# Kernel optimization log

Measured on AMD Instinct MI355X. Metric: run time of the kernel, lower is better.

## Reference

```python
import jax, jax.numpy as jnp
import numpy as np
import math

N, Tp1, V = 256, 33, 10000
D_FEAT, H, W_DIM = 1280, 512, 256
NULL_IDX = 0


def setup_inputs() -> dict:
    key = jax.random.key(0)
    ks = jax.random.split(key, 10)
    feats = jax.random.normal(ks[0], (N, D_FEAT, 4, 4), dtype=jnp.float32)
    captions = jax.random.randint(ks[1], (N, Tp1), 0, V)
    W_proj = jax.random.normal(ks[2], (D_FEAT, H), dtype=jnp.float32) / math.sqrt(D_FEAT)
    b_proj = jnp.zeros((H,), dtype=jnp.float32)
    W_embed = jax.random.normal(ks[3], (V, W_DIM), dtype=jnp.float32) / math.sqrt(V)
    Wx = jax.random.normal(ks[4], (W_DIM, 4 * H), dtype=jnp.float32) / math.sqrt(W_DIM)
    Wh = jax.random.normal(ks[5], (H, 4 * H), dtype=jnp.float32) / math.sqrt(H)
    Wattn = jax.random.normal(ks[6], (H, 4 * H), dtype=jnp.float32) / math.sqrt(H)
    b = jnp.zeros((4 * H,), dtype=jnp.float32)
    W_vocab = jax.random.normal(ks[7], (H, V), dtype=jnp.float32) / math.sqrt(H)
    b_vocab = jnp.zeros((V,), dtype=jnp.float32)
    return {"feats": feats, "captions": captions, "W_proj": W_proj, "b_proj": b_proj,
            "W_embed": W_embed, "Wx": Wx, "Wh": Wh, "Wattn": Wattn, "b": b,
            "W_vocab": W_vocab, "b_vocab": b_vocab}


def _attention_lstm(x, A_flat, h0, Wx, Wh, Wattn, b):
    # x: (N,T,W), A_flat: (N,H,16), h0: (N,H)
    Hh = h0.shape[1]
    scale = 1.0 / math.sqrt(Hh)

    def step(carry, x_t):
        h, c = carry
        # scaled dot-product attention over the 16 spatial positions
        scores = jnp.einsum('nh,nhp->np', h, A_flat) * scale       # (N,16)
        w = jax.nn.softmax(scores, axis=1)
        attn = jnp.einsum('nhp,np->nh', A_flat, w)                 # (N,H)
        a = x_t @ Wx + h @ Wh + b + attn @ Wattn                   # (N,4H)
        i = jax.nn.sigmoid(a[:, 0:Hh])
        f = jax.nn.sigmoid(a[:, Hh:2 * Hh])
        o = jax.nn.sigmoid(a[:, 2 * Hh:3 * Hh])
        g = jnp.tanh(a[:, 3 * Hh:4 * Hh])
        c_next = f * c + i * g
        h_next = o * jnp.tanh(c_next)
        return (h_next, c_next), h_next

    (_, _), hs = jax.lax.scan(step, (h0, h0), jnp.swapaxes(x, 0, 1))
    return jnp.swapaxes(hs, 0, 1)  # (N,T,H)


def reference(feats, captions, W_proj, b_proj, W_embed, Wx, Wh, Wattn, b, W_vocab, b_vocab):
    cap_in = captions[:, :-1]   # (N,T)
    cap_out = captions[:, 1:]   # (N,T)
    # project CNN features per spatial location: (N,Dfeat,4,4) -> (N,H,4,4)
    A = jnp.einsum('ncij,ch->nhij', feats, W_proj) + b_proj[None, :, None, None]
    h0 = A.mean(axis=(2, 3))                     # (N,H); c0 = h0
    A_flat = A.reshape(A.shape[0], A.shape[1], 16)
    x = W_embed[cap_in]                           # (N,T,W)
    h = _attention_lstm(x, A_flat, h0, Wx, Wh, Wattn, b)
    scores = jnp.einsum('nth,hv->ntv', h, W_vocab) + b_vocab   # (N,T,V)
    # temporal softmax loss, sum over tokens (ignoring NULL), averaged over N
    logp = jax.nn.log_softmax(scores, axis=-1)
    nll = -jnp.take_along_axis(logp, cap_out[..., None], axis=-1)[..., 0]  # (N,T)
    mask = (cap_out != NULL_IDX).astype(scores.dtype)
    loss = jnp.sum(nll * mask) / scores.shape[0]
    return loss
```

## Files before the change

### kernel.cpp

```cpp
#include <hip/hip_runtime.h>
#include <hip/hip_bf16.h>

#define NB   256
#define NT   32
#define NV   10000
#define NVP  10240
#define NDF  1280
#define NH   512
#define VT_N 40

typedef short bf16x8 __attribute__((ext_vector_type(8)));
typedef float f32x4  __attribute__((ext_vector_type(4)));
typedef unsigned short u16;

__device__ __forceinline__ float b2f(u16 u) {
    union { unsigned i; float f; } v; v.i = ((unsigned)u) << 16; return v.f;
}
__device__ __forceinline__ u16 f2b(float f) {
    union { float f; unsigned i; } v; v.f = f;
    unsigned r = v.i + 0x7FFF + ((v.i >> 16) & 1);
    return (u16)(r >> 16);
}

__device__ __forceinline__ void gload16(const u16* g, u16* l) {
    __builtin_amdgcn_global_load_lds(
        (const __attribute__((address_space(1))) void*)g,
        (__attribute__((address_space(3))) void*)l, 16, 0, 0);
}

static const size_t B_C     = 0;
static const size_t B_SCP   = B_C     + (size_t)256*512*4;
static const size_t B_PMAX  = B_SCP   + (size_t)2*32*256*16*4;
static const size_t B_PSUM  = B_PMAX  + (size_t)8192*VT_N*4;
static const size_t B_TGT   = B_PSUM  + (size_t)8192*VT_N*4;
static const size_t B_LOSS  = B_TGT   + (size_t)8192*4;
static const size_t B_AB    = B_LOSS  + 16;
static const size_t B_XPB   = B_AB    + (size_t)256*16*512*2;
static const size_t B_HALLB = B_XPB   + (size_t)32*256*2048*2;
static const size_t B_WVT   = B_HALLB + (size_t)32*256*512*2;
static const size_t B_WXT   = B_WVT   + (size_t)10240*512*2;
static const size_t B_WHAT  = B_WXT   + (size_t)2048*256*2;
static const size_t B_HB0   = B_WHAT  + (size_t)2048*1024*2;
static const size_t B_HB1   = B_HB0   + (size_t)256*512*2;
static const size_t B_PREAW = B_HB1   + (size_t)256*512*2;

__global__ __launch_bounds__(256) void tconv_kernel(
    const float* __restrict__ src, u16* __restrict__ dst,
    int K, int N, int Npad, int ldK, int koff)
{
    __shared__ u16 tile[64][65];
    const int k0 = blockIdx.y * 64, n0 = blockIdx.x * 64, tid = threadIdx.x;
#pragma unroll
    for (int i = 0; i < 16; i++) {
        int idx = tid + i * 256;
        int kk = idx >> 6, nn = idx & 63;
        int n = n0 + nn;
        float v = (n < N) ? src[(size_t)(k0 + kk) * N + n] : 0.f;
        tile[kk][nn] = f2b(v);
    }
    __syncthreads();
#pragma unroll
    for (int i = 0; i < 16; i++) {
        int idx = tid + i * 256;
        int nn = idx >> 6, kk = idx & 63;
        int n = n0 + nn;
        if (n < Npad) dst[(size_t)n * ldK + koff + k0 + kk] = tile[kk][nn];
    }
}

__global__ __launch_bounds__(256) void ftrans_kernel(
    const float* __restrict__ feats, u16* __restrict__ fT)
{
    const int cch = blockIdx.x, n = blockIdx.y, tid = threadIdx.x;
    __shared__ u16 lt[64][17];
    const int c0 = cch * 64;
    const int c = tid >> 2, p4 = (tid & 3) * 4;
    float4 v = *(const float4*)(feats + (size_t)n * 20480 + (size_t)(c0 + c) * 16 + p4);
    lt[c][p4] = f2b(v.x); lt[c][p4 + 1] = f2b(v.y);
    lt[c][p4 + 2] = f2b(v.z); lt[c][p4 + 3] = f2b(v.w);
    __syncthreads();
    const int p = tid >> 4, cg = tid & 15;
    ushort4 o;
    o.x = lt[cg * 4 + 0][p]; o.y = lt[cg * 4 + 1][p];
    o.z = lt[cg * 4 + 2][p]; o.w = lt[cg * 4 + 3][p];
    *(ushort4*)(fT + (size_t)(n * 16 + p) * 1280 + c0 + cg * 4) = o;
}

__global__ __launch_bounds__(256) void proj_gemm_kernel(
    const u16* __restrict__ fT, const u16* __restrict__ WpT,
    const float* __restrict__ bp, u16* __restrict__ Ab)
{
    const int ct = blockIdx.x, rt = blockIdx.y;
    const int tid = threadIdx.x, w = tid >> 6, lane = tid & 63;
    const int r0 = rt * 64;
    const int lm = lane & 15, lkq = lane >> 4, lk = lkq * 8;
    const int nbase = ct * 128 + w * 32;

    f32x4 acc[4][2];
#pragma unroll
    for (int mt = 0; mt < 4; mt++)
#pragma unroll
        for (int nt = 0; nt < 2; nt++) acc[mt][nt] = (f32x4){0.f, 0.f, 0.f, 0.f};

    for (int kc = 0; kc < 1280; kc += 32) {
        bf16x8 af[4];
#pragma unroll
        for (int mt = 0; mt < 4; mt++)
            af[mt] = *(const bf16x8*)(fT + (size_t)(r0 + mt * 16 + lm) * 1280 + kc + lk);
#pragma unroll
        for (int nt = 0; nt < 2; nt++) {
            bf16x8 bfg = *(const bf16x8*)(WpT + (size_t)(nbase + nt * 16 + lm) * 1280 + kc + lk);
#pragma unroll
            for (int mt = 0; mt < 4; mt++)
                acc[mt][nt] = __builtin_amdgcn_mfma_f32_16x16x32_bf16(af[mt], bfg, acc[mt][nt], 0, 0, 0);
        }
    }
    float bbv[2];
#pragma unroll
    for (int nt = 0; nt < 2; nt++) bbv[nt] = bp[nbase + nt * 16 + lm];
#pragma unroll
    for (int mt = 0; mt < 4; mt++)
#pragma unroll
        for (int nt = 0; nt < 2; nt++)
#pragma unroll
            for (int r = 0; r < 4; r++) {
                int row = r0 + mt * 16 + lkq * 4 + r;
                int col = nbase + nt * 16 + lm;
                Ab[(size_t)row * 512 + col] = f2b(acc[mt][nt][r] + bbv[nt]);
            }
}

__global__ __launch_bounds__(256) void projmean_kernel(
    const u16* __restrict__ Ab, float* __restrict__ c0, u16* __restrict__ hb0)
{
    const int n = blockIdx.x, tid = threadIdx.x;
    const int col0 = tid, col1 = tid + 256;
    float s0 = 0.f, s1 = 0.f;
#pragma unroll
    for (int p = 0; p < 16; p++) {
        const u16* ap = Ab + ((size_t)n * 16 + p) * 512;
        s0 += b2f(ap[col0]);
        s1 += b2f(ap[col1]);
    }
    s0 *= 0.0625f; s1 *= 0.0625f;
    c0[n * 512 + col0] = s0;  c0[n * 512 + col1] = s1;
    hb0[(size_t)n * 512 + col0] = f2b(s0);
    hb0[(size_t)n * 512 + col1] = f2b(s1);
}

__global__ __launch_bounds__(256) void xp_mfma_kernel(
    const int* __restrict__ caps, const float* __restrict__ We,
    const u16* __restrict__ Wxt, const float* __restrict__ bb,
    u16* __restrict__ xpb)
{
    const int ct = blockIdx.x, rt = blockIdx.y;
    const int tid = threadIdx.x, w = tid >> 6, lane = tid & 63;
    const int r0 = rt * 64;
    const int lm = lane & 15, lkq = lane >> 4, lk = lkq * 8;
    const int nbase = ct * 512 + w * 128;

    int capm[4];
#pragma unroll
    for (int mt = 0; mt < 4; mt++) {
        int row = r0 + mt * 16 + lm;
        capm[mt] = caps[(row >> 5) * 33 + (row & 31)];
    }
    f32x4 acc[4][8];
#pragma unroll
    for (int mt = 0; mt < 4; mt++)
#pragma unroll
        for (int nt = 0; nt < 8; nt++) acc[mt][nt] = (f32x4){0.f, 0.f, 0.f, 0.f};

    for (int kc = 0; kc < 256; kc += 32) {
        bf16x8 af[4];
#pragma unroll
        for (int mt = 0; mt < 4; mt++) {
            const float* ap = We + (size_t)capm[mt] * 256 + kc + lk;
            float4 f0 = *(const float4*)ap;
            float4 f1 = *(const float4*)(ap + 4);
            bf16x8 t;
            t[0] = (short)f2b(f0.x); t[1] = (short)f2b(f0.y);
            t[2] = (short)f2b(f0.z); t[3] = (short)f2b(f0.w);
            t[4] = (short)f2b(f1.x); t[5] = (short)f2b(f1.y);
            t[6] = (short)f2b(f1.z); t[7] = (short)f2b(f1.w);
            af[mt] = t;
        }
#pragma unroll
        for (int nt = 0; nt < 8; nt++) {
            bf16x8 bfg = *(const bf16x8*)(Wxt + (size_t)(nbase + nt * 16 + lm) * 256 + kc + lk);
#pragma unroll
            for (int mt = 0; mt < 4; mt++)
                acc[mt][nt] = __builtin_amdgcn_mfma_f32_16x16x32_bf16(af[mt], bfg, acc[mt][nt], 0, 0, 0);
        }
    }
    float bbv[8];
#pragma unroll
    for (int nt = 0; nt < 8; nt++) bbv[nt] = bb[nbase + nt * 16 + lm];
#pragma unroll
    for (int mt = 0; mt < 4; mt++)
#pragma unroll
        for (int nt = 0; nt < 8; nt++)
#pragma unroll
            for (int r = 0; r < 4; r++) {
                int row = r0 + mt * 16 + lkq * 4 + r;
                int col = nbase + nt * 16 + lm;
                float v = acc[mt][nt][r] + bbv[nt];
                xpb[((size_t)(row & 31) * 256 + (row >> 5)) * 2048 + col] = f2b(v);
            }
}

__global__ __launch_bounds__(256) void preaw_mfma_kernel(
    const u16* __restrict__ Ab, const u16* __restrict__ what,
    u16* __restrict__ preaw)
{
    const int ct = blockIdx.x, rt = blockIdx.y;
    const int tid = threadIdx.x, w = tid >> 6, lane = tid & 63;
    const int r0 = rt * 64;
    const int lm = lane & 15, lkq = lane >> 4, lk = lkq * 8;
    const int nbase = ct * 512 + w * 128;

    f32x4 acc[4][8];
#pragma unroll
    for (int mt = 0; mt < 4; mt++)
#pragma unroll
        for (int nt = 0; nt < 8; nt++) acc[mt][nt] = (f32x4){0.f, 0.f, 0.f, 0.f};

    for (int kc = 0; kc < 512; kc += 32) {
        bf16x8 af[4];
#pragma unroll
        for (int mt = 0; mt < 4; mt++)
            af[mt] = *(const bf16x8*)(Ab + (size_t)(r0 + mt * 16 + lm) * 512 + kc + lk);
#pragma unroll
        for (int nt = 0; nt < 8; nt++) {
            bf16x8 bfg = *(const bf16x8*)(what + (size_t)(nbase + nt * 16 + lm) * 1024 + 512 + kc + lk);
#pragma unroll
            for (int mt = 0; mt < 4; mt++)
                acc[mt][nt] = __builtin_amdgcn_mfma_f32_16x16x32_bf16(af[mt], bfg, acc[mt][nt], 0, 0, 0);
        }
    }
#pragma unroll
    for (int mt = 0; mt < 4; mt++) {
        int nIdx = (r0 >> 4) + mt;
#pragma unroll
        for (int nt = 0; nt < 8; nt++) {
            int col = nbase + nt * 16 + lm;
            ushort4 o;
            o.x = f2b(acc[mt][nt][0]); o.y = f2b(acc[mt][nt][1]);
            o.z = f2b(acc[mt][nt][2]); o.w = f2b(acc[mt][nt][3]);
            *(ushort4*)(preaw + (size_t)nIdx * 32768 + (size_t)col * 16 + lkq * 4) = o;
        }
    }
}

__global__ __launch_bounds__(64) void score_init_kernel(
    const u16* __restrict__ hb0, const u16* __restrict__ Ab,
    float* __restrict__ scp)
{
    const int n = blockIdx.x, lane = threadIdx.x;
    const u16* hp = hb0 + (size_t)n * 512 + lane * 8;
    ushort4 h0 = *(const ushort4*)hp, h1 = *(const ushort4*)(hp + 4);
    float hv0 = b2f(h0.x), hv1 = b2f(h0.y), hv2 = b2f(h0.z), hv3 = b2f(h0.w);
    float hv4 = b2f(h1.x), hv5 = b2f(h1.y), hv6 = b2f(h1.z), hv7 = b2f(h1.w);
    float mine = 0.f;
#pragma unroll
    for (int p = 0; p < 16; p++) {
        const u16* ap = Ab + (size_t)n * 8192 + p * 512 + lane * 8;
        ushort4 a0 = *(const ushort4*)ap, a1 = *(const ushort4*)(ap + 4);
        float s = hv0*b2f(a0.x) + hv1*b2f(a0.y) + hv2*b2f(a0.z) + hv3*b2f(a0.w)
                + hv4*b2f(a1.x) + hv5*b2f(a1.y) + hv6*b2f(a1.z) + hv7*b2f(a1.w);
#pragma unroll
        for (int mask = 1; mask <= 32; mask <<= 1) s += __shfl_xor(s, mask, 64);
        if (lane == p) mine = s;
    }
    if (lane < 16) scp[n * 16 + lane] = mine;
    for (int i = lane; i < 31 * 16; i += 64)
        scp[(1 + (i >> 4)) * 4096 + n * 16 + (i & 15)] = 0.f;
}

__global__ __launch_bounds__(256, 2) void gates_fused_kernel(
    const u16* __restrict__ hb_in, const float* __restrict__ scp_in,
    const u16* __restrict__ what, const u16* __restrict__ preaw,
    const u16* __restrict__ xpt, const u16* __restrict__ Ab,
    float* __restrict__ c, u16* __restrict__ hb_out,
    u16* __restrict__ hallbt, float* __restrict__ scp_out)
{
    const int rt = blockIdx.x, cg = blockIdx.y;
    const int tid = threadIdx.x, ty = tid >> 6, lane = tid & 63;
    const int lm = lane & 15, lkq = lane >> 4, lk = lkq * 8;
    const int r0 = rt * 16, hc0 = cg * 16;

    __shared__ u16 hs[16 * 520];
    __shared__ float sred[16][17];
    __shared__ float wts[16][17];
    __shared__ float gred[4][16][18];
    __shared__ u16 hnew[16][16];

    const int col = ty * 512 + hc0 + lm;

    const u16* brow = what + (size_t)col * 1024 + lk;
    bf16x8 bfa[16];
#pragma unroll
    for (int i = 0; i < 16; i++) bfa[i] = *(const bf16x8*)(brow + i * 32);

    ushort4 pwv[4][4];
#pragma unroll
    for (int r = 0; r < 4; r++) {
        const u16* pp = preaw + (size_t)(r0 + lkq * 4 + r) * 32768 + (size_t)col * 16;
#pragma unroll
        for (int j = 0; j < 4; j++) pwv[r][j] = *(const ushort4*)(pp + j * 4);
    }
    u16 xpw[4];
#pragma unroll
    for (int r = 0; r < 4; r++) xpw[r] = xpt[(size_t)(r0 + lkq * 4 + r) * 2048 + col];

    const int rg = lkq * 4 + ty;
    const int idxg = (r0 + rg) * 512 + hc0 + lm;
    float cin = c[idxg];

    const int rs = tid >> 4, ps = tid & 15;
    ushort4 abv[4];
    {
        const u16* ap = Ab + (size_t)(r0 + rs) * 8192 + ps * 512 + hc0;
#pragma unroll
        for (int j = 0; j < 4; j++) abv[j] = *(const ushort4*)(ap + j * 4);
    }

#pragma unroll
    for (int i = 0; i < 8; i++) {
        int fid = tid + i * 256;
        int rr = fid >> 7, c4 = fid & 127;
        *(ushort4*)&hs[rr * 520 + c4 * 4] =
            *(const ushort4*)(hb_in + (size_t)(r0 + rr) * 512 + c4 * 4);
    }
    {
        float s = 0.f;
#pragma unroll
        for (int g = 0; g < 32; g++) s += scp_in[g * 4096 + (r0 + rs) * 16 + ps];
        sred[rs][ps] = s * 0.04419417382415922f;
    }
    __syncthreads();
    {
        float m = -1e30f;
#pragma unroll
        for (int q = 0; q < 16; q++) m = fmaxf(m, sred[rs][q]);
        float su = 0.f;
#pragma unroll
        for (int q = 0; q < 16; q++) su += __expf(sred[rs][q] - m);
        wts[rs][ps] = __expf(sred[rs][ps] - m) / su;
    }
    f32x4 acc = (f32x4){0.f, 0.f, 0.f, 0.f};
    const u16* arow = &hs[lm * 520 + lk];
#pragma unroll
    for (int i = 0; i < 16; i++) {
        bf16x8 af = *(const bf16x8*)(arow + i * 32);
        acc = __builtin_amdgcn_mfma_f32_16x16x32_bf16(af, bfa[i], acc, 0, 0, 0);
    }
    __syncthreads();
#pragma unroll
    for (int r = 0; r < 4; r++) {
        const int rl = lkq * 4 + r;
        float s = acc[r] + b2f(xpw[r]);
#pragma unroll
        for (int j = 0; j < 4; j++) {
            s += wts[rl][j * 4 + 0] * b2f(pwv[r][j].x);
            s += wts[rl][j * 4 + 1] * b2f(pwv[r][j].y);
            s += wts[rl][j * 4 + 2] * b2f(pwv[r][j].z);
            s += wts[rl][j * 4 + 3] * b2f(pwv[r][j].w);
        }
        gred[ty][rl][lm] = s;
    }
    __syncthreads();
    {
        float ai  = gred[0][rg][lm];
        float af_ = gred[1][rg][lm];
        float ao  = gred[2][rg][lm];
        float ag  = gred[3][rg][lm];
        float ig = 1.f / (1.f + __expf(-ai));
        float fg = 1.f / (1.f + __expf(-af_));
        float og = 1.f / (1.f + __expf(-ao));
        float gv = tanhf(ag);
        float cn = fg * cin + ig * gv;
        float hn = og * tanhf(cn);
        c[idxg] = cn;
        u16 hbv = f2b(hn);
        hb_out[idxg] = hbv;
        hallbt[idxg] = hbv;
        hnew[rg][lm] = hbv;
    }
    __syncthreads();
    {
        float s = 0.f;
#pragma unroll
        for (int j = 0; j < 4; j++) {
            s += b2f(hnew[rs][j * 4 + 0]) * b2f(abv[j].x);
            s += b2f(hnew[rs][j * 4 + 1]) * b2f(abv[j].y);
            s += b2f(hnew[rs][j * 4 + 2]) * b2f(abv[j].z);
            s += b2f(hnew[rs][j * 4 + 3]) * b2f(abv[j].w);
        }
        scp_out[cg * 4096 + (r0 + rs) * 16 + ps] = s;
    }
}

__global__ __launch_bounds__(512) void vocab_mfma_kernel(
    const u16* __restrict__ hallb, const u16* __restrict__ Wvt,
    const float* __restrict__ bv, const int* __restrict__ caps,
    float* __restrict__ pmax, float* __restrict__ psum, float* __restrict__ tgt)
{
    const int ct = blockIdx.x, rt = blockIdx.y;
    const int tid = threadIdx.x, w = tid >> 6, lane = tid & 63;
    const int wr = w >> 2, wc = w & 3;
    const int r0 = rt * 128, c0 = ct * 256;
    const int lm = lane & 15, lkq = lane >> 4;
    const int swz = lkq ^ ((lm >> 1) & 3);

    __shared__ u16 As[3][512 * 8];
    __shared__ u16 Bs[3][1024 * 8];
    __shared__ int tvs[128];
    __shared__ float cm[128][4], cs[128][4];

    if (tid < 128) {
        int row = r0 + tid;
        tvs[tid] = caps[(row & 255) * 33 + (row >> 8) + 1];
    }

    f32x4 acc[4][4];
#pragma unroll
    for (int mt = 0; mt < 4; mt++)
#pragma unroll
        for (int nt = 0; nt < 4; nt++) acc[mt][nt] = (f32x4){0.f, 0.f, 0.f, 0.f};

    const int sA = w * 64 + lane;
    const int rA = sA >> 2, kA = (sA & 3) ^ ((rA >> 1) & 3);
    const u16* gA = hallb + (size_t)(r0 + rA) * 512 + kA * 8;
    const int sB0 = w * 64 + lane, sB1 = sB0 + 512;
    const int cB0 = sB0 >> 2, kB0 = (sB0 & 3) ^ ((cB0 >> 1) & 3);
    const int cB1 = sB1 >> 2, kB1 = (sB1 & 3) ^ ((cB1 >> 1) & 3);
    const u16* gB0 = Wvt + (size_t)(c0 + cB0) * 512 + kB0 * 8;
    const u16* gB1 = Wvt + (size_t)(c0 + cB1) * 512 + kB1 * 8;

    auto stage = [&](int buf, int kc) {
        gload16(gA + kc, &As[buf][w * 512]);
        gload16(gB0 + kc, &Bs[buf][w * 512]);
        gload16(gB1 + kc, &Bs[buf][(w + 8) * 512]);
    };
    auto compute = [&](int buf) {
        bf16x8 af[4], bfr[4];
#pragma unroll
        for (int mt = 0; mt < 4; mt++)
            af[mt] = *(const bf16x8*)&As[buf][((wr * 64 + mt * 16 + lm) * 4 + swz) * 8];
#pragma unroll
        for (int nt = 0; nt < 4; nt++)
            bfr[nt] = *(const bf16x8*)&Bs[buf][((wc * 64 + nt * 16 + lm) * 4 + swz) * 8];
#pragma unroll
        for (int nt = 0; nt < 4; nt++)
#pragma unroll
            for (int mt = 0; mt < 4; mt++)
                acc[mt][nt] = __builtin_amdgcn_mfma_f32_16x16x32_bf16(af[mt], bfr[nt], acc[mt][nt], 0, 0, 0);
    };

    stage(0, 0);
    stage(1, 32);
#pragma unroll 1
    for (int t = 0; t < 16; ++t) {
        if (t + 2 < 16) stage((t + 2) % 3, (t + 2) * 32);
        if (t < 14)       asm volatile("s_waitcnt vmcnt(6)" ::: "memory");
        else if (t == 14) asm volatile("s_waitcnt vmcnt(3)" ::: "memory");
        else              asm volatile("s_waitcnt vmcnt(0)" ::: "memory");
        __builtin_amdgcn_s_barrier();
        compute(t % 3);
        __builtin_amdgcn_s_barrier();
    }

    float bvv[4]; bool vld[4];
#pragma unroll
    for (int nt = 0; nt < 4; nt++) {
        int col = c0 + wc * 64 + nt * 16 + lm;
        vld[nt] = (col < NV);
        bvv[nt] = vld[nt] ? bv[col] : 0.f;
    }
#pragma unroll
    for (int mt = 0; mt < 4; mt++)
#pragma unroll
        for (int r = 0; r < 4; r++) {
            int rloc = wr * 64 + mt * 16 + lkq * 4 + r;
            int row = r0 + rloc;
            int tv = tvs[rloc];
            float vals[4]; float m = -1e30f;
#pragma unroll
            for (int nt = 0; nt < 4; nt++) {
                int col = c0 + wc * 64 + nt * 16 + lm;
                float v = vld[nt] ? (acc[mt][nt][r] + bvv[nt]) : -1e30f;
                vals[nt] = v;
                m = fmaxf(m, v);
                if (col == tv) tgt[row] = v;
            }
#pragma unroll
            for (int mask = 1; mask <= 8; mask <<= 1) m = fmaxf(m, __shfl_xor(m, mask, 64));
            float s = 0.f;
#pragma unroll
            for (int nt = 0; nt < 4; nt++) s += __expf(vals[nt] - m);
#pragma unroll
            for (int mask = 1; mask <= 8; mask <<= 1) s += __shfl_xor(s, mask, 64);
            if (lm == 0) { cm[rloc][wc] = m; cs[rloc][wc] = s; }
        }
    __syncthreads();
    if (tid < 128) {
        float M = -1e30f;
#pragma unroll
        for (int q = 0; q < 4; q++) M = fmaxf(M, cm[tid][q]);
        float S = 0.f;
#pragma unroll
        for (int q = 0; q < 4; q++) S += cs[tid][q] * __expf(cm[tid][q] - M);
        int row = r0 + tid;
        pmax[row * VT_N + ct] = M;
        psum[row * VT_N + ct] = S;
    }
}

__global__ __launch_bounds__(256) void loss_reduce_kernel(
    const float* __restrict__ pmax, const float* __restrict__ psum,
    const float* __restrict__ tgt, const int* __restrict__ caps,
    float* __restrict__ loss)
{
    const int row = blockIdx.x * 256 + threadIdx.x;
    float nll = 0.f;
    const int t = row >> 8, n = row & 255;
    const int tv = caps[n * 33 + t + 1];
    if (tv != 0) {
        float M = -1e30f;
#pragma unroll
        for (int vt = 0; vt < VT_N; vt++) M = fmaxf(M, pmax[row * VT_N + vt]);
        float S = 0.f;
#pragma unroll
        for (int vt = 0; vt < VT_N; vt++) S += psum[row * VT_N + vt] * __expf(pmax[row * VT_N + vt] - M);
        nll = logf(S) + M - tgt[row];
    }
#pragma unroll
    for (int off = 32; off; off >>= 1) nll += __shfl_down(nll, off, 64);
    __shared__ float r4[4];
    if ((threadIdx.x & 63) == 0) r4[threadIdx.x >> 6] = nll;
    __syncthreads();
    if (threadIdx.x == 0)
        atomicAdd(loss, (r4[0] + r4[1] + r4[2] + r4[3]) * (1.f / 256.f));
}

__global__ void finalize_kernel(const float* __restrict__ loss, float* __restrict__ out)
{
    if (threadIdx.x == 0 && blockIdx.x == 0) out[0] = loss[0];
}

extern "C" void kernel_launch(void* const* d_in, const int* in_sizes, int n_in,
                              void* d_out, int out_size, void* d_ws, size_t ws_size,
                              hipStream_t stream) {
    const float* feats = (const float*)d_in[0];
    const int*   caps  = (const int*)d_in[1];
    const float* Wp    = (const float*)d_in[2];
    const float* bp    = (const float*)d_in[3];
    const float* We    = (const float*)d_in[4];
    const float* Wx    = (const float*)d_in[5];
    const float* Wh    = (const float*)d_in[6];
    const float* Wattn = (const float*)d_in[7];
    const float* bb    = (const float*)d_in[8];
    const float* Wv    = (const float*)d_in[9];
    const float* bv    = (const float*)d_in[10];

    char* ws = (char*)d_ws;
    float* c     = (float*)(ws + B_C);
    float* scp0  = (float*)(ws + B_SCP);
    float* scp1  = scp0 + (size_t)32 * 4096;
    float* pmax  = (float*)(ws + B_PMAX);
    float* psum  = (float*)(ws + B_PSUM);
    float* tgt   = (float*)(ws + B_TGT);
    float* loss  = (float*)(ws + B_LOSS);
    u16*   Ab    = (u16*)(ws + B_AB);
    u16*   xpb   = (u16*)(ws + B_XPB);
    u16*   hallb = (u16*)(ws + B_HALLB);
    u16*   wvt   = (u16*)(ws + B_WVT);
    u16*   wxt   = (u16*)(ws + B_WXT);
    u16*   what  = (u16*)(ws + B_WHAT);
    u16*   hb[2] = { (u16*)(ws + B_HB0), (u16*)(ws + B_HB1) };
    u16*   preaw = (u16*)(ws + B_PREAW);
    u16*   fT    = wvt;
    u16*   WpT   = xpb;

    hipMemsetAsync(loss, 0, sizeof(float), stream);

    ftrans_kernel<<<dim3(20, 256), 256, 0, stream>>>(feats, fT);
    tconv_kernel<<<dim3(8, 20), 256, 0, stream>>>(Wp, WpT, 1280, 512, 512, 1280, 0);
    proj_gemm_kernel<<<dim3(4, 64), 256, 0, stream>>>(fT, WpT, bp, Ab);
    projmean_kernel<<<256, 256, 0, stream>>>(Ab, c, hb[0]);

    tconv_kernel<<<dim3(160, 8), 256, 0, stream>>>(Wv, wvt, 512, NV, NVP, 512, 0);
    tconv_kernel<<<dim3(32, 4),  256, 0, stream>>>(Wx, wxt, 256, 2048, 2048, 256, 0);
    tconv_kernel<<<dim3(32, 8),  256, 0, stream>>>(Wh, what, 512, 2048, 2048, 1024, 0);
    tconv_kernel<<<dim3(32, 8),  256, 0, stream>>>(Wattn, what, 512, 2048, 2048, 1024, 512);
    xp_mfma_kernel<<<dim3(4, 128), 256, 0, stream>>>(caps, We, wxt, bb, xpb);
    preaw_mfma_kernel<<<dim3(4, 64), 256, 0, stream>>>(Ab, what, preaw);
    score_init_kernel<<<256, 64, 0, stream>>>(hb[0], Ab, scp0);

    for (int t = 0; t < NT; t++) {
        const int in = t & 1;
        gates_fused_kernel<<<dim3(16, 32), 256, 0, stream>>>(
            hb[in], in ? scp1 : scp0, what, preaw,
            xpb + (size_t)t * 524288, Ab, c,
            hb[1 - in], hallb + (size_t)t * 131072,
            in ? scp0 : scp1);
    }

    vocab_mfma_kernel<<<dim3(VT_N, 64), 512, 0, stream>>>(
        hallb, wvt, bv, caps, pmax, psum, tgt);
    loss_reduce_kernel<<<32, 256, 0, stream>>>(pmax, psum, tgt, caps, loss);
    finalize_kernel<<<1, 64, 0, stream>>>(loss, (float*)d_out);
}
```

Before: 753.3 us.

## Enlarge vocab GEMM tile to 256x256 with split-k-chunk buffering and single barrier

The vocab projection kernel now computes a 256-row by 256-column tile per block instead of 128x256, so each wave holds 8x4 MFMA accumulators and the grid halves along rows. Each K step of 32 is split into two 4096-element LDS slots per operand, giving six rotating slots. Prefetch is issued after the barrier, which removes the second barrier per iteration. The aim is more reuse of each loaded fragment and less synchronisation. The cost is more accumulator registers per thread, which launch_bounds(512,2) must fit, and fewer blocks to spread across the GPU.

```diff
diff --git a/kernel.cpp b/kernel.cpp
--- a/kernel.cpp
+++ b/kernel.cpp
@@ -401,7 +401,7 @@
     }
 }
 
-__global__ __launch_bounds__(512) void vocab_mfma_kernel(
+__global__ __launch_bounds__(512, 2) void vocab_mfma_kernel(
     const u16* __restrict__ hallb, const u16* __restrict__ Wvt,
     const float* __restrict__ bv, const int* __restrict__ caps,
     float* __restrict__ pmax, float* __restrict__ psum, float* __restrict__ tgt)
@@ -409,66 +409,67 @@
     const int ct = blockIdx.x, rt = blockIdx.y;
     const int tid = threadIdx.x, w = tid >> 6, lane = tid & 63;
     const int wr = w >> 2, wc = w & 3;
-    const int r0 = rt * 128, c0 = ct * 256;
+    const int r0 = rt * 256, c0 = ct * 256;
     const int lm = lane & 15, lkq = lane >> 4;
     const int swz = lkq ^ ((lm >> 1) & 3);
 
-    __shared__ u16 As[3][512 * 8];
-    __shared__ u16 Bs[3][1024 * 8];
-    __shared__ int tvs[128];
-    __shared__ float cm[128][4], cs[128][4];
-
-    if (tid < 128) {
+    __shared__ u16 As[6][4096];
+    __shared__ u16 Bs[6][4096];
+    __shared__ int tvs[256];
+    __shared__ float cm[256][4], cs[256][4];
+
+    if (tid < 256) {
         int row = r0 + tid;
         tvs[tid] = caps[(row & 255) * 33 + (row >> 8) + 1];
     }
 
-    f32x4 acc[4][4];
-#pragma unroll
-    for (int mt = 0; mt < 4; mt++)
+    f32x4 acc[8][4];
+#pragma unroll
+    for (int mt = 0; mt < 8; mt++)
 #pragma unroll
         for (int nt = 0; nt < 4; nt++) acc[mt][nt] = (f32x4){0.f, 0.f, 0.f, 0.f};
 
-    const int sA = w * 64 + lane;
-    const int rA = sA >> 2, kA = (sA & 3) ^ ((rA >> 1) & 3);
-    const u16* gA = hallb + (size_t)(r0 + rA) * 512 + kA * 8;
-    const int sB0 = w * 64 + lane, sB1 = sB0 + 512;
-    const int cB0 = sB0 >> 2, kB0 = (sB0 & 3) ^ ((cB0 >> 1) & 3);
-    const int cB1 = sB1 >> 2, kB1 = (sB1 & 3) ^ ((cB1 >> 1) & 3);
-    const u16* gB0 = Wvt + (size_t)(c0 + cB0) * 512 + kB0 * 8;
-    const u16* gB1 = Wvt + (size_t)(c0 + cB1) * 512 + kB1 * 8;
-
-    auto stage = [&](int buf, int kc) {
-        gload16(gA + kc, &As[buf][w * 512]);
-        gload16(gB0 + kc, &Bs[buf][w * 512]);
-        gload16(gB1 + kc, &Bs[buf][(w + 8) * 512]);
+    const int rr = tid >> 2;
+    const int kq = (tid & 3) ^ ((rr >> 1) & 3);
+    const u16* gA0 = hallb + (size_t)(r0 + rr) * 512 + kq * 8;
+    const u16* gA1 = hallb + (size_t)(r0 + 128 + rr) * 512 + kq * 8;
+    const u16* gB0 = Wvt + (size_t)(c0 + rr) * 512 + kq * 8;
+    const u16* gB1 = Wvt + (size_t)(c0 + 128 + rr) * 512 + kq * 8;
+
+    auto stage = [&](int t) {
+        const int kb = t * 32;
+        const int s0 = (2 * t) % 6, s1 = (2 * t + 1) % 6;
+        gload16(gA0 + kb, &As[s0][w * 512]);
+        gload16(gA1 + kb, &As[s1][w * 512]);
+        gload16(gB0 + kb, &Bs[s0][w * 512]);
+        gload16(gB1 + kb, &Bs[s1][w * 512]);
     };
-    auto compute = [&](int buf) {
-        bf16x8 af[4], bfr[4];
-#pragma unroll
-        for (int mt = 0; mt < 4; mt++)
-            af[mt] = *(const bf16x8*)&As[buf][((wr * 64 + mt * 16 + lm) * 4 + swz) * 8];
-#pragma unroll
-        for (int nt = 0; nt < 4; nt++)
-            bfr[nt] = *(const bf16x8*)&Bs[buf][((wc * 64 + nt * 16 + lm) * 4 + swz) * 8];
-#pragma unroll
-        for (int nt = 0; nt < 4; nt++)
-#pragma unroll
-            for (int mt = 0; mt < 4; mt++)
-                acc[mt][nt] = __builtin_amdgcn_mfma_f32_16x16x32_bf16(af[mt], bfr[nt], acc[mt][nt], 0, 0, 0);
-    };
-
-    stage(0, 0);
-    stage(1, 32);
+
+    stage(0); stage(1);
 #pragma unroll 1
     for (int t = 0; t < 16; ++t) {
-        if (t + 2 < 16) stage((t + 2) % 3, (t + 2) * 32);
-        if (t < 14)       asm volatile("s_waitcnt vmcnt(6)" ::: "memory");
-        else if (t == 14) asm volatile("s_waitcnt vmcnt(3)" ::: "memory");
-        else              asm volatile("s_waitcnt vmcnt(0)" ::: "memory");
+        if (t < 15) asm volatile("s_waitcnt vmcnt(4)" ::: "memory");
+        else        asm volatile("s_waitcnt vmcnt(0)" ::: "memory");
         __builtin_amdgcn_s_barrier();
-        compute(t % 3);
-        __builtin_amdgcn_s_barrier();
+        if (t + 2 < 16) stage(t + 2);
+        const int sa = (2 * t + wr) % 6;
+        const int sb = (2 * t + (wc >> 1)) % 6;
+        bf16x8 af[8], bfr[4];
+#pragma unroll
+        for (int mt = 0; mt < 8; mt++) {
+            int ra = mt * 16 + lm;
+            af[mt] = *(const bf16x8*)&As[sa][(ra * 4 + swz) * 8];
+        }
+#pragma unroll
+        for (int nt = 0; nt < 4; nt++) {
+            int rb = (wc & 1) * 64 + nt * 16 + lm;
+            bfr[nt] = *(const bf16x8*)&Bs[sb][(rb * 4 + swz) * 8];
+        }
+#pragma unroll
+        for (int nt = 0; nt < 4; nt++)
+#pragma unroll
+            for (int mt = 0; mt < 8; mt++)
+                acc[mt][nt] = __builtin_amdgcn_mfma_f32_16x16x32_bf16(af[mt], bfr[nt], acc[mt][nt], 0, 0, 0);
     }
 
     float bvv[4]; bool vld[4];
@@ -479,10 +480,10 @@
         bvv[nt] = vld[nt] ? bv[col] : 0.f;
     }
 #pragma unroll
-    for (int mt = 0; mt < 4; mt++)
+    for (int mt = 0; mt < 8; mt++)
 #pragma unroll
         for (int r = 0; r < 4; r++) {
-            int rloc = wr * 64 + mt * 16 + lkq * 4 + r;
+            int rloc = wr * 128 + mt * 16 + lkq * 4 + r;
             int row = r0 + rloc;
             int tv = tvs[rloc];
             float vals[4]; float m = -1e30f;
@@ -504,7 +505,7 @@
             if (lm == 0) { cm[rloc][wc] = m; cs[rloc][wc] = s; }
         }
     __syncthreads();
-    if (tid < 128) {
+    if (tid < 256) {
         float M = -1e30f;
 #pragma unroll
         for (int q = 0; q < 4; q++) M = fmaxf(M, cm[tid][q]);
@@ -607,7 +608,7 @@
             in ? scp0 : scp1);
     }
 
-    vocab_mfma_kernel<<<dim3(VT_N, 64), 512, 0, stream>>>(
+    vocab_mfma_kernel<<<dim3(VT_N, 32), 512, 0, stream>>>(
         hallb, wvt, bv, caps, pmax, psum, tgt);
     loss_reduce_kernel<<<32, 256, 0, stream>>>(pmax, psum, tgt, caps, loss);
     finalize_kernel<<<1, 64, 0, stream>>>(loss, (float*)d_out);
```

New measurement: 786.2 us. 1.04x slower.
